# Performance work log

Hardware: AMD Instinct MI355X
Metric: run time of the kernel (lower is better)

## Reference

```python
import jax, jax.numpy as jnp
import numpy as np

B, S, D_MODEL, H = 2, 2048, 512, 8
DH = D_MODEL // H  # dim per head
NEG_INF = 1e9


def setup_inputs() -> dict:
    key = jax.random.key(0)
    ks = jax.random.split(key, 8)
    sc = 0.05
    return {
        "query": jax.random.normal(ks[0], (B, S, D_MODEL), jnp.float32),
        "key": jax.random.normal(ks[1], (B, S, D_MODEL), jnp.float32),
        "value": jax.random.normal(ks[2], (B, S, D_MODEL), jnp.float32),
        "mask": jnp.zeros((B, 1, S, S), jnp.float32),
        "wq": jax.random.normal(ks[3], (D_MODEL, D_MODEL), jnp.float32) * sc,
        "bq": jnp.zeros((D_MODEL,), jnp.float32),
        "wk": jax.random.normal(ks[4], (D_MODEL, D_MODEL), jnp.float32) * sc,
        "bk": jnp.zeros((D_MODEL,), jnp.float32),
        "wv": jax.random.normal(ks[5], (D_MODEL, D_MODEL), jnp.float32) * sc,
        "bv": jnp.zeros((D_MODEL,), jnp.float32),
        "wo": jax.random.normal(ks[6], (D_MODEL, D_MODEL), jnp.float32) * sc,
        "bo": jnp.zeros((D_MODEL,), jnp.float32),
    }


def _split_heads(x):
    # (B, S, D_MODEL) -> (B, H, S, DH)
    b, s, _ = x.shape
    return x.reshape(b, s, H, DH).transpose(0, 2, 1, 3)


def reference(query, key, value, mask, wq, bq, wk, bk, wv, bv, wo, bo):
    q = _split_heads(query @ wq + bq)
    k = _split_heads(key @ wk + bk)
    v = _split_heads(value @ wv + bv)
    # scaled dot-product attention; full (B, H, S, S) scores as in original
    scores = jnp.einsum("bhqd,bhkd->bhqk", q, k) / jnp.sqrt(jnp.float32(DH))
    scores = scores + mask * (-NEG_INF)
    weights = jax.nn.softmax(scores, axis=-1)  # dropout inactive (rate=0 / eval)
    attn = jnp.einsum("bhqk,bhkd->bhqd", weights, v)
    # merge heads: (B, H, S, DH) -> (B, S, D_MODEL)
    b = attn.shape[0]
    merged = attn.transpose(0, 2, 1, 3).reshape(b, -1, D_MODEL)
    return merged @ wo + bo
```

## Files before the change

### kernel.cpp

```cpp
#include <hip/hip_runtime.h>
#include <hip/hip_bf16.h>

typedef unsigned short u16;
typedef unsigned int u32;
typedef __bf16 bf16x8 __attribute__((ext_vector_type(8)));
typedef float f32x4 __attribute__((ext_vector_type(4)));
typedef u16 u16x8 __attribute__((ext_vector_type(8)));
typedef u32 u32x2 __attribute__((ext_vector_type(2)));

#define S_LEN 2048
#define DMODEL 512
#define NHEAD 8
#define DHEAD 64
#define QSCALE 0.1803368801111204f
#define MASKC 1.4426950409e9f
#define RESCALE_THR 8.0f

static __device__ __forceinline__ u16 f2bf(float f) {
    union { float f; unsigned u; } cv; cv.f = f;
    unsigned u = cv.u;
    return (u16)((u + 0x7fffu + ((u >> 16) & 1u)) >> 16);
}
static __device__ __forceinline__ u32 pk2bf(float a, float b) {
    union { __hip_bfloat162 h; u32 u; } cv;
    float2 f2; f2.x = a; f2.y = b;
    cv.h = __float22bfloat162_rn(f2);
    return cv.u;
}
static __device__ __forceinline__ bf16x8 ld8(const u16* p) {
    return *(const bf16x8*)p;
}
static __device__ __forceinline__ float fmax3(float a, float b, float c) {
    return __builtin_fmaxf(__builtin_fmaxf(a, b), c);
}

__global__ __launch_bounds__(256) void prep_kernel(
    const float* __restrict__ q, const float* __restrict__ k, const float* __restrict__ v,
    const float* __restrict__ w0, const float* __restrict__ w1,
    const float* __restrict__ w2, const float* __restrict__ w3,
    const float* __restrict__ mask,
    u16* __restrict__ Aqkv, u16* __restrict__ wtall, int* __restrict__ flags) {
    const int p = blockIdx.x;
    const int tid = threadIdx.x;
    __shared__ float t[32][33];
    __shared__ int wred[4];
    if (p < 3072) {
        const int z = p >> 10, px = p & 1023;
        const float* in = (z == 0) ? q : (z == 1) ? k : v;
        u16* o = Aqkv + (long)z * 2097152;
        long i = ((long)px * 256 + tid) * 8;
        f32x4 a = *(const f32x4*)(in + i);
        f32x4 b = *(const f32x4*)(in + i + 4);
        u16x8 r;
#pragma unroll
        for (int j = 0; j < 4; ++j) { r[j] = f2bf(a[j]); r[4 + j] = f2bf(b[j]); }
        *(u16x8*)(o + i) = r;
    } else if (p < 4096) {
        const int p2 = p - 3072;
        const int z = p2 >> 8, rem = p2 & 255, by = rem >> 4, bx = rem & 15;
        const float* in = (z == 0) ? w0 : (z == 1) ? w1 : (z == 2) ? w2 : w3;
        u16* o = wtall + (long)(((z + 1) & 3)) * 262144;
        const int tx = tid & 31, ty = tid >> 5;
#pragma unroll
        for (int i = 0; i < 4; ++i)
            t[ty + 8 * i][tx] = in[(by * 32 + ty + 8 * i) * DMODEL + bx * 32 + tx];
        __syncthreads();
#pragma unroll
        for (int i = 0; i < 4; ++i)
            o[(bx * 32 + ty + 8 * i) * DMODEL + by * 32 + tx] = f2bf(t[tx][ty + 8 * i]);
    } else {
        const int bid = p - 4096;
        const int b = bid >> 10, qt = (bid >> 5) & 31, kt = bid & 31;
        const int r = tid >> 2, cs = tid & 3;
        const float* mp = mask + ((long)(b * S_LEN + qt * 64 + r)) * S_LEN + kt * 64 + cs * 16;
        int nz = 0;
#pragma unroll
        for (int j = 0; j < 4; ++j) {
            f32x4 a = *(const f32x4*)(mp + j * 4);
            nz |= (a[0] != 0.f) | (a[1] != 0.f) | (a[2] != 0.f) | (a[3] != 0.f);
        }
        unsigned long long ball = __ballot(nz);
        if ((tid & 63) == 0) wred[tid >> 6] = (ball != 0ull) ? 1 : 0;
        __syncthreads();
        if (tid == 0) flags[bid] = wred[0] | wred[1] | wred[2] | wred[3];
    }
}

template <bool F32OUT, int TM>
static __device__ __forceinline__ void gemm_body(const u16* __restrict__ A,
                                                 const u16* __restrict__ Wt,
                                                 const float* __restrict__ bias,
                                                 void* __restrict__ Cp, float oscale,
                                                 bool vtout, int bx, int by) {
    const int lane = threadIdx.x & 63;
    const int wave = threadIdx.x >> 6;
    const int wr = wave >> 1, wc = wave & 1;
    const int m0 = by * (TM * 32) + wr * (TM * 16);
    const int n0 = bx * 64 + wc * 32;
    const int cidx = lane & 15;
    const int kg = lane >> 4;

    const u16* aptr[TM];
    const u16* bptr[2];
#pragma unroll
    for (int t = 0; t < TM; ++t)
        aptr[t] = A + (long)(m0 + t * 16 + cidx) * DMODEL + kg * 8;
#pragma unroll
    for (int t = 0; t < 2; ++t)
        bptr[t] = Wt + (long)(n0 + t * 16 + cidx) * DMODEL + kg * 8;

    const f32x4 fz = {0.f, 0.f, 0.f, 0.f};
    f32x4 acc[TM][2];
#pragma unroll
    for (int i = 0; i < TM; ++i)
#pragma unroll
        for (int j = 0; j < 2; ++j) acc[i][j] = fz;

#pragma unroll 4
    for (int k0 = 0; k0 < 512; k0 += 32) {
        bf16x8 a[TM], b[2];
#pragma unroll
        for (int t = 0; t < TM; ++t) a[t] = ld8(aptr[t] + k0);
#pragma unroll
        for (int t = 0; t < 2; ++t) b[t] = ld8(bptr[t] + k0);
#pragma unroll
        for (int i = 0; i < TM; ++i)
#pragma unroll
            for (int j = 0; j < 2; ++j)
                acc[i][j] = __builtin_amdgcn_mfma_f32_16x16x32_bf16(a[i], b[j], acc[i][j], 0, 0, 0);
    }

    if (vtout) {
        const int bb = m0 >> 11;
#pragma unroll
        for (int j = 0; j < 2; ++j) {
            int col = n0 + j * 16 + cidx;
            float bv = bias[col];
            u16* vt = (u16*)Cp + (((long)(bb * 8 + (col >> 6))) * 64 + (col & 63)) * S_LEN;
#pragma unroll
            for (int i = 0; i < TM; ++i) {
                int s = (m0 + i * 16 + kg * 4) & (S_LEN - 1);
                u32x2 d;
                d[0] = pk2bf(acc[i][j][0] + bv, acc[i][j][1] + bv);
                d[1] = pk2bf(acc[i][j][2] + bv, acc[i][j][3] + bv);
                *(u32x2*)(vt + s) = d;
            }
        }
        return;
    }

#pragma unroll
    for (int j = 0; j < 2; ++j) {
        int col = n0 + j * 16 + cidx;
        float bv = bias[col];
#pragma unroll
        for (int i = 0; i < TM; ++i) {
#pragma unroll
            for (int r = 0; r < 4; ++r) {
                int row = m0 + i * 16 + kg * 4 + r;
                float val = (acc[i][j][r] + bv) * oscale;
                if (F32OUT) {
                    ((float*)Cp)[(long)row * DMODEL + col] = val;
                } else {
                    ((u16*)Cp)[(long)row * DMODEL + col] = f2bf(val);
                }
            }
        }
    }
}

static __device__ __forceinline__ void xcd_swizzle(int gridX, int gridY, int& bx, int& by) {
    const int flat = blockIdx.x + gridX * blockIdx.y;
    const int xcd = flat & 7;
    const int j = flat >> 3;
    by = xcd * (gridY >> 3) + j / gridX;
    bx = j % gridX;
}

__global__ __launch_bounds__(256) void qkv_gemm_kernel(
    const u16* __restrict__ Aqkv,
    const u16* __restrict__ wtall,
    const float* __restrict__ bq, const float* __restrict__ bk, const float* __restrict__ bv,
    u16* __restrict__ Q, u16* __restrict__ K, u16* __restrict__ Vt) {
    const u16* A = Aqkv + (long)blockIdx.z * 2097152;
    const u16* W = wtall + (long)(blockIdx.z + 1) * 262144;
    const float* b;
    u16* C;
    float sc = 1.f;
    bool vt = false;
    if (blockIdx.z == 0) { b = bq; C = Q; sc = QSCALE; }
    else if (blockIdx.z == 1) { b = bk; C = K; }
    else { b = bv; C = Vt; vt = true; }
    int bx, by;
    xcd_swizzle(8, 32, bx, by);
    gemm_body<false, 4>(A, W, b, C, sc, vt, bx, by);
}

__global__ __launch_bounds__(256) void out_gemm_kernel(const u16* __restrict__ A,
                                                       const u16* __restrict__ Wt,
                                                       const float* __restrict__ bias,
                                                       float* __restrict__ C) {
    int bx, by;
    xcd_swizzle(8, 64, bx, by);
    gemm_body<true, 2>(A, Wt, bias, C, 1.f, false, bx, by);
}

__global__ __launch_bounds__(256) void attn_kernel(const u16* __restrict__ Q,
                                                   const u16* __restrict__ K,
                                                   const u16* __restrict__ Vt,
                                                   const float* __restrict__ mask,
                                                   const int* __restrict__ flags,
                                                   u16* __restrict__ Ab) {
    const int tid = threadIdx.x;
    const int lane = tid & 63;
    const int wave = tid >> 6;
    const int cidx = lane & 15;
    const int kg = lane >> 4;
    const int bh = blockIdx.y;
    const int b = bh >> 3, h = bh & 7;
    const int q0 = blockIdx.x * 64 + wave * 16;

    __shared__ u16 kt_lds[2][64 * 64];
    __shared__ u16 vt_lds[2][64 * 64];
    __shared__ u16 p_lds[4][16 * 64];
    u16* pw = p_lds[wave];

    const long qbase = ((long)(b * S_LEN + q0 + cidx)) * DMODEL + h * DHEAD + kg * 8;
    bf16x8 aq0 = ld8(Q + qbase);
    bf16x8 aq1 = ld8(Q + qbase + 32);

    bf16x8 onesf;
    {
        u16x8 t8;
        u16 ob = (cidx == 0) ? (u16)0x3F80 : (u16)0;
#pragma unroll
        for (int j = 0; j < 8; ++j) t8[j] = ob;
        onesf = *(bf16x8*)&t8;
    }

    const f32x4 fz = {0.f, 0.f, 0.f, 0.f};
    f32x4 acc[4];
#pragma unroll
    for (int nt = 0; nt < 4; ++nt) acc[nt] = fz;
    f32x4 accL = fz;
    float mrow = -1e30f;

    const int krow0 = tid >> 3, kseg0 = tid & 7;
    const int krow1 = krow0 + 32;
    const u16* kgbase = K + ((long)(b * S_LEN)) * DMODEL + h * DHEAD;
    const u16* vgbase = Vt + ((long)bh * DHEAD) * S_LEN;
    const int kd0 = krow0 * 64 + (((kseg0 ^ (krow0 & 7))) << 3);
    const int kd1 = krow1 * 64 + (((kseg0 ^ (krow1 & 7))) << 3);
    const int* flagrow = flags + b * 1024 + blockIdx.x * 32;
    const int NIT = S_LEN / 64;

    const u16* kp0 = kgbase + (long)krow0 * DMODEL + kseg0 * 8;
    const u16* kp1 = kgbase + (long)krow1 * DMODEL + kseg0 * 8;
    const u16* vp0 = vgbase + (long)krow0 * S_LEN + kseg0 * 8;
    const u16* vp1 = vgbase + (long)krow1 * S_LEN + kseg0 * 8;

    u16x8 rk0 = *(const u16x8*)kp0;
    u16x8 rk1 = *(const u16x8*)kp1;
    u16x8 rv0 = *(const u16x8*)vp0;
    u16x8 rv1 = *(const u16x8*)vp1;
    *(u16x8*)&kt_lds[0][kd0] = rk0;
    *(u16x8*)&kt_lds[0][kd1] = rk1;
    *(u16x8*)&vt_lds[0][kd0] = rv0;
    *(u16x8*)&vt_lds[0][kd1] = rv1;
    rk0 = *(const u16x8*)(kp0 + 64 * DMODEL);
    rk1 = *(const u16x8*)(kp1 + 64 * DMODEL);
    rv0 = *(const u16x8*)(vp0 + 64);
    rv1 = *(const u16x8*)(vp1 + 64);
    __syncthreads();

    for (int it = 0; it < NIT; ++it) {
        const int cur = it & 1;
        if (it + 1 < NIT) {
            u16* kn = kt_lds[cur ^ 1];
            u16* vn = vt_lds[cur ^ 1];
            *(u16x8*)&kn[kd0] = rk0;
            *(u16x8*)&kn[kd1] = rk1;
            *(u16x8*)&vn[kd0] = rv0;
            *(u16x8*)&vn[kd1] = rv1;
            if (it + 2 < NIT) {
                const int t2 = (it + 2) * 64;
                rk0 = *(const u16x8*)(kp0 + (long)t2 * DMODEL);
                rk1 = *(const u16x8*)(kp1 + (long)t2 * DMODEL);
                rv0 = *(const u16x8*)(vp0 + t2);
                rv1 = *(const u16x8*)(vp1 + t2);
            }
        }
        const int flg = flagrow[it];
        const u16* kb = kt_lds[cur];
        const u16* vb = vt_lds[cur];

        f32x4 sacc[4];
#pragma unroll
        for (int ct = 0; ct < 4; ++ct) sacc[ct] = fz;
        __builtin_amdgcn_s_setprio(1);
#pragma unroll
        for (int ct = 0; ct < 4; ++ct) {
            int r = ct * 16 + cidx;
            bf16x8 kv0 = ld8(&kb[r * 64 + ((kg ^ (r & 7)) << 3)]);
            bf16x8 kv1 = ld8(&kb[r * 64 + (((4 ^ kg) ^ (r & 7)) << 3)]);
            sacc[ct] = __builtin_amdgcn_mfma_f32_16x16x32_bf16(kv0, aq0, sacc[ct], 0, 0, 0);
            sacc[ct] = __builtin_amdgcn_mfma_f32_16x16x32_bf16(kv1, aq1, sacc[ct], 0, 0, 0);
        }
        __builtin_amdgcn_s_setprio(0);
        if (flg) {
            const float* mb = mask + ((long)(b * S_LEN + q0 + cidx)) * S_LEN + it * 64 + kg * 4;
#pragma unroll
            for (int ct = 0; ct < 4; ++ct) {
                f32x4 mv = *(const f32x4*)(mb + ct * 16);
#pragma unroll
                for (int r = 0; r < 4; ++r) sacc[ct][r] -= MASKC * mv[r];
            }
        }
        float t0 = fmax3(sacc[0][0], sacc[0][1], sacc[0][2]);
        float t1 = fmax3(sacc[0][3], sacc[1][0], sacc[1][1]);
        float t2 = fmax3(sacc[1][2], sacc[1][3], sacc[2][0]);
        float t3 = fmax3(sacc[2][1], sacc[2][2], sacc[2][3]);
        float t4 = fmax3(sacc[3][0], sacc[3][1], sacc[3][2]);
        float mxl = __builtin_fmaxf(fmax3(fmax3(t0, t1, t2), t3, t4), sacc[3][3]);
        if (__any(mxl > mrow + RESCALE_THR)) {
            float mx = fmaxf(mxl, __shfl_xor(mxl, 16));
            mx = fmaxf(mx, __shfl_xor(mx, 32));
            float mnew = fmaxf(mrow, mx);
            float alpha = __builtin_amdgcn_exp2f(mrow - mnew);
            mrow = mnew;
            accL = accL * alpha;
#pragma unroll
            for (int nt = 0; nt < 4; ++nt) acc[nt] = acc[nt] * alpha;
        }
#pragma unroll
        for (int ct = 0; ct < 4; ++ct)
#pragma unroll
            for (int r = 0; r < 4; ++r)
                sacc[ct][r] = __builtin_amdgcn_exp2f(sacc[ct][r] - mrow);
#pragma unroll
        for (int ct = 0; ct < 4; ++ct) {
            u32x2 d;
            d[0] = pk2bf(sacc[ct][0], sacc[ct][1]);
            d[1] = pk2bf(sacc[ct][2], sacc[ct][3]);
            int blk = 2 * ct + (kg >> 1);
            *(u32x2*)&pw[cidx * 64 + ((blk ^ (cidx & 7)) << 3) + (kg & 1) * 4] = d;
        }
        bf16x8 pf0 = ld8(&pw[cidx * 64 + ((kg ^ (cidx & 7)) << 3)]);
        bf16x8 pf1 = ld8(&pw[cidx * 64 + (((4 ^ kg) ^ (cidx & 7)) << 3)]);
        __builtin_amdgcn_s_setprio(1);
#pragma unroll
        for (int nt = 0; nt < 4; ++nt) {
            int rr = nt * 16 + cidx;
            bf16x8 v0 = ld8(&vb[rr * 64 + ((kg ^ (rr & 7)) << 3)]);
            bf16x8 v1 = ld8(&vb[rr * 64 + (((4 ^ kg) ^ (rr & 7)) << 3)]);
            acc[nt] = __builtin_amdgcn_mfma_f32_16x16x32_bf16(v0, pf0, acc[nt], 0, 0, 0);
            acc[nt] = __builtin_amdgcn_mfma_f32_16x16x32_bf16(v1, pf1, acc[nt], 0, 0, 0);
        }
        accL = __builtin_amdgcn_mfma_f32_16x16x32_bf16(onesf, pf0, accL, 0, 0, 0);
        accL = __builtin_amdgcn_mfma_f32_16x16x32_bf16(onesf, pf1, accL, 0, 0, 0);
        __builtin_amdgcn_s_setprio(0);
        __syncthreads();
    }
    float Lb = __shfl(accL[0], cidx);
    float invL = 1.f / Lb;
    const long abase = ((long)(b * S_LEN + q0 + cidx)) * DMODEL + h * DHEAD;
#pragma unroll
    for (int nt = 0; nt < 4; ++nt) {
        u32x2 d;
        d[0] = pk2bf(acc[nt][0] * invL, acc[nt][1] * invL);
        d[1] = pk2bf(acc[nt][2] * invL, acc[nt][3] * invL);
        *(u32x2*)(Ab + abase + nt * 16 + kg * 4) = d;
    }
}

extern "C" void kernel_launch(void* const* d_in, const int* in_sizes, int n_in,
                              void* d_out, int out_size, void* d_ws, size_t ws_size,
                              hipStream_t stream) {
    const float* q_in = (const float*)d_in[0];
    const float* k_in = (const float*)d_in[1];
    const float* v_in = (const float*)d_in[2];
    const float* mask = (const float*)d_in[3];
    const float* wq = (const float*)d_in[4];
    const float* bq = (const float*)d_in[5];
    const float* wk = (const float*)d_in[6];
    const float* bk = (const float*)d_in[7];
    const float* wv = (const float*)d_in[8];
    const float* bv = (const float*)d_in[9];
    const float* wo = (const float*)d_in[10];
    const float* bo = (const float*)d_in[11];

    u16* ws = (u16*)d_ws;
    u16* Qb = ws;
    u16* Kb = Qb + 2097152;
    u16* Vt = Kb + 2097152;
    u16* wtall = Vt + 2097152;
    u16* Sreg = wtall + 4 * 262144;
    u16* Ab = Sreg + 3 * 2097152;
    int* mflags = (int*)(Ab + 2097152);

    prep_kernel<<<6144, 256, 0, stream>>>(q_in, k_in, v_in, wq, wk, wv, wo, mask,
                                          Sreg, wtall, mflags);
    qkv_gemm_kernel<<<dim3(8, 32, 3), 256, 0, stream>>>(Sreg, wtall, bq, bk, bv, Qb, Kb, Vt);
    attn_kernel<<<dim3(32, 16), 256, 0, stream>>>(Qb, Kb, Vt, mask, mflags, Ab);
    out_gemm_kernel<<<dim3(8, 64), 256, 0, stream>>>(Ab, wtall, bo, (float*)d_out);
}
```

Baseline: 202.2 us.

## Fuse fp32-to-bf16 input conversion into QKV GEMM, swizzle and unroll attention

Drops the separate activation conversion pass from the prep kernel. The QKV GEMM now reads fp32 inputs directly and packs them to bf16 in registers, removing a bf16 write and re-read of the activations. The attention kernel also remaps block indices in an XCD-aware way and unrolls its tile loop by two with a macro, giving constant double-buffer indices. The trade-off is that the GEMM loads twice the bytes per A fragment and does the conversion redundantly across the N-tile blocks.

```diff
diff --git a/kernel.cpp b/kernel.cpp
--- a/kernel.cpp
+++ b/kernel.cpp
@@ -7,6 +7,7 @@
 typedef float f32x4 __attribute__((ext_vector_type(4)));
 typedef u16 u16x8 __attribute__((ext_vector_type(8)));
 typedef u32 u32x2 __attribute__((ext_vector_type(2)));
+typedef u32 u32x4 __attribute__((ext_vector_type(4)));
 
 #define S_LEN 2048
 #define DMODEL 512
@@ -30,34 +31,29 @@
 static __device__ __forceinline__ bf16x8 ld8(const u16* p) {
     return *(const bf16x8*)p;
 }
+static __device__ __forceinline__ bf16x8 ld8f(const float* p) {
+    f32x4 a = *(const f32x4*)p;
+    f32x4 b = *(const f32x4*)(p + 4);
+    u32x4 w;
+    w[0] = pk2bf(a[0], a[1]); w[1] = pk2bf(a[2], a[3]);
+    w[2] = pk2bf(b[0], b[1]); w[3] = pk2bf(b[2], b[3]);
+    union { u32x4 u; bf16x8 h; } cv; cv.u = w; return cv.h;
+}
 static __device__ __forceinline__ float fmax3(float a, float b, float c) {
     return __builtin_fmaxf(__builtin_fmaxf(a, b), c);
 }
 
 __global__ __launch_bounds__(256) void prep_kernel(
-    const float* __restrict__ q, const float* __restrict__ k, const float* __restrict__ v,
     const float* __restrict__ w0, const float* __restrict__ w1,
     const float* __restrict__ w2, const float* __restrict__ w3,
     const float* __restrict__ mask,
-    u16* __restrict__ Aqkv, u16* __restrict__ wtall, int* __restrict__ flags) {
+    u16* __restrict__ wtall, int* __restrict__ flags) {
     const int p = blockIdx.x;
     const int tid = threadIdx.x;
     __shared__ float t[32][33];
     __shared__ int wred[4];
-    if (p < 3072) {
-        const int z = p >> 10, px = p & 1023;
-        const float* in = (z == 0) ? q : (z == 1) ? k : v;
-        u16* o = Aqkv + (long)z * 2097152;
-        long i = ((long)px * 256 + tid) * 8;
-        f32x4 a = *(const f32x4*)(in + i);
-        f32x4 b = *(const f32x4*)(in + i + 4);
-        u16x8 r;
-#pragma unroll
-        for (int j = 0; j < 4; ++j) { r[j] = f2bf(a[j]); r[4 + j] = f2bf(b[j]); }
-        *(u16x8*)(o + i) = r;
-    } else if (p < 4096) {
-        const int p2 = p - 3072;
-        const int z = p2 >> 8, rem = p2 & 255, by = rem >> 4, bx = rem & 15;
+    if (p < 1024) {
+        const int z = p >> 8, rem = p & 255, by = rem >> 4, bx = rem & 15;
         const float* in = (z == 0) ? w0 : (z == 1) ? w1 : (z == 2) ? w2 : w3;
         u16* o = wtall + (long)(((z + 1) & 3)) * 262144;
         const int tx = tid & 31, ty = tid >> 5;
@@ -69,7 +65,7 @@
         for (int i = 0; i < 4; ++i)
             o[(bx * 32 + ty + 8 * i) * DMODEL + by * 32 + tx] = f2bf(t[tx][ty + 8 * i]);
     } else {
-        const int bid = p - 4096;
+        const int bid = p - 1024;
         const int b = bid >> 10, qt = (bid >> 5) & 31, kt = bid & 31;
         const int r = tid >> 2, cs = tid & 3;
         const float* mp = mask + ((long)(b * S_LEN + qt * 64 + r)) * S_LEN + kt * 64 + cs * 16;
@@ -83,6 +79,49 @@
         if ((tid & 63) == 0) wred[tid >> 6] = (ball != 0ull) ? 1 : 0;
         __syncthreads();
         if (tid == 0) flags[bid] = wred[0] | wred[1] | wred[2] | wred[3];
+    }
+}
+
+template <bool F32OUT, int TM>
+static __device__ __forceinline__ void store_c(f32x4 (&acc)[TM][2],
+                                               const float* __restrict__ bias,
+                                               void* __restrict__ Cp, float oscale,
+                                               bool vtout, int m0, int n0, int cidx, int kg) {
+    if (vtout) {
+        const int bb = m0 >> 11;
+#pragma unroll
+        for (int j = 0; j < 2; ++j) {
+            int col = n0 + j * 16 + cidx;
+            float bv = bias[col];
+            u16* vt = (u16*)Cp + (((long)(bb * 8 + (col >> 6))) * 64 + (col & 63)) * S_LEN;
+#pragma unroll
+            for (int i = 0; i < TM; ++i) {
+                int s = (m0 + i * 16 + kg * 4) & (S_LEN - 1);
+                u32x2 d;
+                d[0] = pk2bf(acc[i][j][0] + bv, acc[i][j][1] + bv);
+                d[1] = pk2bf(acc[i][j][2] + bv, acc[i][j][3] + bv);
+                *(u32x2*)(vt + s) = d;
+            }
+        }
+        return;
+    }
+#pragma unroll
+    for (int j = 0; j < 2; ++j) {
+        int col = n0 + j * 16 + cidx;
+        float bv = bias[col];
+#pragma unroll
+        for (int i = 0; i < TM; ++i) {
+#pragma unroll
+            for (int r = 0; r < 4; ++r) {
+                int row = m0 + i * 16 + kg * 4 + r;
+                float val = (acc[i][j][r] + bv) * oscale;
+                if (F32OUT) {
+                    ((float*)Cp)[(long)row * DMODEL + col] = val;
+                } else {
+                    ((u16*)Cp)[(long)row * DMODEL + col] = f2bf(val);
+                }
+            }
+        }
     }
 }
 
@@ -129,44 +168,53 @@
             for (int j = 0; j < 2; ++j)
                 acc[i][j] = __builtin_amdgcn_mfma_f32_16x16x32_bf16(a[i], b[j], acc[i][j], 0, 0, 0);
     }
-
-    if (vtout) {
-        const int bb = m0 >> 11;
-#pragma unroll
-        for (int j = 0; j < 2; ++j) {
-            int col = n0 + j * 16 + cidx;
-            float bv = bias[col];
-            u16* vt = (u16*)Cp + (((long)(bb * 8 + (col >> 6))) * 64 + (col & 63)) * S_LEN;
-#pragma unroll
-            for (int i = 0; i < TM; ++i) {
-                int s = (m0 + i * 16 + kg * 4) & (S_LEN - 1);
-                u32x2 d;
-                d[0] = pk2bf(acc[i][j][0] + bv, acc[i][j][1] + bv);
-                d[1] = pk2bf(acc[i][j][2] + bv, acc[i][j][3] + bv);
-                *(u32x2*)(vt + s) = d;
-            }
-        }
-        return;
-    }
-
-#pragma unroll
-    for (int j = 0; j < 2; ++j) {
-        int col = n0 + j * 16 + cidx;
-        float bv = bias[col];
-#pragma unroll
-        for (int i = 0; i < TM; ++i) {
-#pragma unroll
-            for (int r = 0; r < 4; ++r) {
-                int row = m0 + i * 16 + kg * 4 + r;
-                float val = (acc[i][j][r] + bv) * oscale;
-                if (F32OUT) {
-                    ((float*)Cp)[(long)row * DMODEL + col] = val;
-                } else {
-                    ((u16*)Cp)[(long)row * DMODEL + col] = f2bf(val);
-                }
-            }
-        }
-    }
+    store_c<F32OUT, TM>(acc, bias, Cp, oscale, vtout, m0, n0, cidx, kg);
+}
+
+template <int TM>
+static __device__ __forceinline__ void gemm_body_af32(const float* __restrict__ A,
+                                                      const u16* __restrict__ Wt,
+                                                      const float* __restrict__ bias,
+                                                      void* __restrict__ Cp, float oscale,
+                                                      bool vtout, int bx, int by) {
+    const int lane = threadIdx.x & 63;
+    const int wave = threadIdx.x >> 6;
+    const int wr = wave >> 1, wc = wave & 1;
+    const int m0 = by * (TM * 32) + wr * (TM * 16);
+    const int n0 = bx * 64 + wc * 32;
+    const int cidx = lane & 15;
+    const int kg = lane >> 4;
+
+    const float* aptr[TM];
+    const u16* bptr[2];
+#pragma unroll
+    for (int t = 0; t < TM; ++t)
+        aptr[t] = A + (long)(m0 + t * 16 + cidx) * DMODEL + kg * 8;
+#pragma unroll
+    for (int t = 0; t < 2; ++t)
+        bptr[t] = Wt + (long)(n0 + t * 16 + cidx) * DMODEL + kg * 8;
+
+    const f32x4 fz = {0.f, 0.f, 0.f, 0.f};
+    f32x4 acc[TM][2];
+#pragma unroll
+    for (int i = 0; i < TM; ++i)
+#pragma unroll
+        for (int j = 0; j < 2; ++j) acc[i][j] = fz;
+
+#pragma unroll 2
+    for (int k0 = 0; k0 < 512; k0 += 32) {
+        bf16x8 a[TM], b[2];
+#pragma unroll
+        for (int t = 0; t < TM; ++t) a[t] = ld8f(aptr[t] + k0);
+#pragma unroll
+        for (int t = 0; t < 2; ++t) b[t] = ld8(bptr[t] + k0);
+#pragma unroll
+        for (int i = 0; i < TM; ++i)
+#pragma unroll
+            for (int j = 0; j < 2; ++j)
+                acc[i][j] = __builtin_amdgcn_mfma_f32_16x16x32_bf16(a[i], b[j], acc[i][j], 0, 0, 0);
+    }
+    store_c<false, TM>(acc, bias, Cp, oscale, vtout, m0, n0, cidx, kg);
 }
 
 static __device__ __forceinline__ void xcd_swizzle(int gridX, int gridY, int& bx, int& by) {
@@ -178,11 +226,11 @@
 }
 
 __global__ __launch_bounds__(256) void qkv_gemm_kernel(
-    const u16* __restrict__ Aqkv,
+    const float* __restrict__ Aq, const float* __restrict__ Ak, const float* __restrict__ Av,
     const u16* __restrict__ wtall,
     const float* __restrict__ bq, const float* __restrict__ bk, const float* __restrict__ bv,
     u16* __restrict__ Q, u16* __restrict__ K, u16* __restrict__ Vt) {
-    const u16* A = Aqkv + (long)blockIdx.z * 2097152;
+    const float* A = (blockIdx.z == 0) ? Aq : (blockIdx.z == 1) ? Ak : Av;
     const u16* W = wtall + (long)(blockIdx.z + 1) * 262144;
     const float* b;
     u16* C;
@@ -193,7 +241,7 @@
     else { b = bv; C = Vt; vt = true; }
     int bx, by;
     xcd_swizzle(8, 32, bx, by);
-    gemm_body<false, 4>(A, W, b, C, sc, vt, bx, by);
+    gemm_body_af32<4>(A, W, b, C, sc, vt, bx, by);
 }
 
 __global__ __launch_bounds__(256) void out_gemm_kernel(const u16* __restrict__ A,
@@ -216,9 +264,12 @@
     const int wave = tid >> 6;
     const int cidx = lane & 15;
     const int kg = lane >> 4;
-    const int bh = blockIdx.y;
+    const int flat = blockIdx.x + 32 * blockIdx.y;
+    const int F = (flat & 7) * 64 + (flat >> 3);
+    const int qt = F & 31;
+    const int bh = F >> 5;
     const int b = bh >> 3, h = bh & 7;
-    const int q0 = blockIdx.x * 64 + wave * 16;
+    const int q0 = qt * 64 + wave * 16;
 
     __shared__ u16 kt_lds[2][64 * 64];
     __shared__ u16 vt_lds[2][64 * 64];
@@ -251,7 +302,7 @@
     const u16* vgbase = Vt + ((long)bh * DHEAD) * S_LEN;
     const int kd0 = krow0 * 64 + (((kseg0 ^ (krow0 & 7))) << 3);
     const int kd1 = krow1 * 64 + (((kseg0 ^ (krow1 & 7))) << 3);
-    const int* flagrow = flags + b * 1024 + blockIdx.x * 32;
+    const int* flagrow = flags + b * 1024 + qt * 32;
     const int NIT = S_LEN / 64;
 
     const u16* kp0 = kgbase + (long)krow0 * DMODEL + kseg0 * 8;
@@ -273,94 +324,100 @@
     rv1 = *(const u16x8*)(vp1 + 64);
     __syncthreads();
 
-    for (int it = 0; it < NIT; ++it) {
-        const int cur = it & 1;
-        if (it + 1 < NIT) {
-            u16* kn = kt_lds[cur ^ 1];
-            u16* vn = vt_lds[cur ^ 1];
-            *(u16x8*)&kn[kd0] = rk0;
-            *(u16x8*)&kn[kd1] = rk1;
-            *(u16x8*)&vn[kd0] = rv0;
-            *(u16x8*)&vn[kd1] = rv1;
-            if (it + 2 < NIT) {
-                const int t2 = (it + 2) * 64;
-                rk0 = *(const u16x8*)(kp0 + (long)t2 * DMODEL);
-                rk1 = *(const u16x8*)(kp1 + (long)t2 * DMODEL);
-                rv0 = *(const u16x8*)(vp0 + t2);
-                rv1 = *(const u16x8*)(vp1 + t2);
-            }
-        }
-        const int flg = flagrow[it];
-        const u16* kb = kt_lds[cur];
-        const u16* vb = vt_lds[cur];
-
-        f32x4 sacc[4];
-#pragma unroll
-        for (int ct = 0; ct < 4; ++ct) sacc[ct] = fz;
-        __builtin_amdgcn_s_setprio(1);
-#pragma unroll
-        for (int ct = 0; ct < 4; ++ct) {
-            int r = ct * 16 + cidx;
-            bf16x8 kv0 = ld8(&kb[r * 64 + ((kg ^ (r & 7)) << 3)]);
-            bf16x8 kv1 = ld8(&kb[r * 64 + (((4 ^ kg) ^ (r & 7)) << 3)]);
-            sacc[ct] = __builtin_amdgcn_mfma_f32_16x16x32_bf16(kv0, aq0, sacc[ct], 0, 0, 0);
-            sacc[ct] = __builtin_amdgcn_mfma_f32_16x16x32_bf16(kv1, aq1, sacc[ct], 0, 0, 0);
-        }
-        __builtin_amdgcn_s_setprio(0);
-        if (flg) {
-            const float* mb = mask + ((long)(b * S_LEN + q0 + cidx)) * S_LEN + it * 64 + kg * 4;
-#pragma unroll
-            for (int ct = 0; ct < 4; ++ct) {
-                f32x4 mv = *(const f32x4*)(mb + ct * 16);
-#pragma unroll
-                for (int r = 0; r < 4; ++r) sacc[ct][r] -= MASKC * mv[r];
-            }
-        }
-        float t0 = fmax3(sacc[0][0], sacc[0][1], sacc[0][2]);
-        float t1 = fmax3(sacc[0][3], sacc[1][0], sacc[1][1]);
-        float t2 = fmax3(sacc[1][2], sacc[1][3], sacc[2][0]);
-        float t3 = fmax3(sacc[2][1], sacc[2][2], sacc[2][3]);
-        float t4 = fmax3(sacc[3][0], sacc[3][1], sacc[3][2]);
-        float mxl = __builtin_fmaxf(fmax3(fmax3(t0, t1, t2), t3, t4), sacc[3][3]);
-        if (__any(mxl > mrow + RESCALE_THR)) {
-            float mx = fmaxf(mxl, __shfl_xor(mxl, 16));
-            mx = fmaxf(mx, __shfl_xor(mx, 32));
-            float mnew = fmaxf(mrow, mx);
-            float alpha = __builtin_amdgcn_exp2f(mrow - mnew);
-            mrow = mnew;
-            accL = accL * alpha;
-#pragma unroll
-            for (int nt = 0; nt < 4; ++nt) acc[nt] = acc[nt] * alpha;
-        }
-#pragma unroll
-        for (int ct = 0; ct < 4; ++ct)
-#pragma unroll
-            for (int r = 0; r < 4; ++r)
-                sacc[ct][r] = __builtin_amdgcn_exp2f(sacc[ct][r] - mrow);
-#pragma unroll
-        for (int ct = 0; ct < 4; ++ct) {
-            u32x2 d;
-            d[0] = pk2bf(sacc[ct][0], sacc[ct][1]);
-            d[1] = pk2bf(sacc[ct][2], sacc[ct][3]);
-            int blk = 2 * ct + (kg >> 1);
-            *(u32x2*)&pw[cidx * 64 + ((blk ^ (cidx & 7)) << 3) + (kg & 1) * 4] = d;
-        }
-        bf16x8 pf0 = ld8(&pw[cidx * 64 + ((kg ^ (cidx & 7)) << 3)]);
-        bf16x8 pf1 = ld8(&pw[cidx * 64 + (((4 ^ kg) ^ (cidx & 7)) << 3)]);
-        __builtin_amdgcn_s_setprio(1);
-#pragma unroll
-        for (int nt = 0; nt < 4; ++nt) {
-            int rr = nt * 16 + cidx;
-            bf16x8 v0 = ld8(&vb[rr * 64 + ((kg ^ (rr & 7)) << 3)]);
-            bf16x8 v1 = ld8(&vb[rr * 64 + (((4 ^ kg) ^ (rr & 7)) << 3)]);
-            acc[nt] = __builtin_amdgcn_mfma_f32_16x16x32_bf16(v0, pf0, acc[nt], 0, 0, 0);
-            acc[nt] = __builtin_amdgcn_mfma_f32_16x16x32_bf16(v1, pf1, acc[nt], 0, 0, 0);
-        }
-        accL = __builtin_amdgcn_mfma_f32_16x16x32_bf16(onesf, pf0, accL, 0, 0, 0);
-        accL = __builtin_amdgcn_mfma_f32_16x16x32_bf16(onesf, pf1, accL, 0, 0, 0);
-        __builtin_amdgcn_s_setprio(0);
-        __syncthreads();
-    }
+#define ATTN_TILE(IT, CUR)                                                                 \
+    {                                                                                      \
+        if ((IT) + 1 < NIT) {                                                              \
+            u16* kn = kt_lds[(CUR) ^ 1];                                                   \
+            u16* vn = vt_lds[(CUR) ^ 1];                                                   \
+            *(u16x8*)&kn[kd0] = rk0;                                                       \
+            *(u16x8*)&kn[kd1] = rk1;                                                       \
+            *(u16x8*)&vn[kd0] = rv0;                                                       \
+            *(u16x8*)&vn[kd1] = rv1;                                                       \
+            if ((IT) + 2 < NIT) {                                                          \
+                const int t2 = ((IT) + 2) * 64;                                            \
+                rk0 = *(const u16x8*)(kp0 + (long)t2 * DMODEL);                            \
+                rk1 = *(const u16x8*)(kp1 + (long)t2 * DMODEL);                            \
+                rv0 = *(const u16x8*)(vp0 + t2);                                           \
+                rv1 = *(const u16x8*)(vp1 + t2);                                           \
+            }                                                                              \
+        }                                                                                  \
+        const int flg = flagrow[(IT)];                                                     \
+        const u16* kb = kt_lds[(CUR)];                                                     \
+        const u16* vb = vt_lds[(CUR)];                                                     \
+        f32x4 sacc[4];                                                                     \
+        _Pragma("unroll")                                                                  \
+        for (int ct = 0; ct < 4; ++ct) sacc[ct] = fz;                                      \
+        __builtin_amdgcn_s_setprio(1);                                                     \
+        _Pragma("unroll")                                                                  \
+        for (int ct = 0; ct < 4; ++ct) {                                                   \
+            int r = ct * 16 + cidx;                                                        \
+            bf16x8 kv0 = ld8(&kb[r * 64 + ((kg ^ (r & 7)) << 3)]);                         \
+            bf16x8 kv1 = ld8(&kb[r * 64 + (((4 ^ kg) ^ (r & 7)) << 3)]);                   \
+            sacc[ct] = __builtin_amdgcn_mfma_f32_16x16x32_bf16(kv0, aq0, sacc[ct], 0, 0, 0); \
+            sacc[ct] = __builtin_amdgcn_mfma_f32_16x16x32_bf16(kv1, aq1, sacc[ct], 0, 0, 0); \
+        }                                                                                  \
+        __builtin_amdgcn_s_setprio(0);                                                     \
+        if (flg) {                                                                         \
+            const float* mb = mask + ((long)(b * S_LEN + q0 + cidx)) * S_LEN + (IT) * 64 + kg * 4; \
+            _Pragma("unroll")                                                              \
+            for (int ct = 0; ct < 4; ++ct) {                                               \
+                f32x4 mv = *(const f32x4*)(mb + ct * 16);                                  \
+                _Pragma("unroll")                                                          \
+                for (int r = 0; r < 4; ++r) sacc[ct][r] -= MASKC * mv[r];                  \
+            }                                                                              \
+        }                                                                                  \
+        float t0 = fmax3(sacc[0][0], sacc[0][1], sacc[0][2]);                              \
+        float t1 = fmax3(sacc[0][3], sacc[1][0], sacc[1][1]);                              \
+        float t2 = fmax3(sacc[1][2], sacc[1][3], sacc[2][0]);                              \
+        float t3 = fmax3(sacc[2][1], sacc[2][2], sacc[2][3]);                              \
+        float t4 = fmax3(sacc[3][0], sacc[3][1], sacc[3][2]);                              \
+        float mxl = __builtin_fmaxf(fmax3(fmax3(t0, t1, t2), t3, t4), sacc[3][3]);         \
+        if (__any(mxl > mrow + RESCALE_THR)) {                                             \
+            float mx = fmaxf(mxl, __shfl_xor(mxl, 16));                                    \
+            mx = fmaxf(mx, __shfl_xor(mx, 32));                                            \
+            float mnew = fmaxf(mrow, mx);                                                  \
+            float alpha = __builtin_amdgcn_exp2f(mrow - mnew);                             \
+            mrow = mnew;                                                                   \
+            accL = accL * alpha;                                                           \
+            _Pragma("unroll")                                                              \
+            for (int nt = 0; nt < 4; ++nt) acc[nt] = acc[nt] * alpha;                      \
+        }                                                                                  \
+        _Pragma("unroll")                                                                  \
+        for (int ct = 0; ct < 4; ++ct)                                                     \
+            _Pragma("unroll")                                                              \
+            for (int r = 0; r < 4; ++r)                                                    \
+                sacc[ct][r] = __builtin_amdgcn_exp2f(sacc[ct][r] - mrow);                  \
+        _Pragma("unroll")                                                                  \
+        for (int ct = 0; ct < 4; ++ct) {                                                   \
+            u32x2 d;                                                                       \
+            d[0] = pk2bf(sacc[ct][0], sacc[ct][1]);                                        \
+            d[1] = pk2bf(sacc[ct][2], sacc[ct][3]);                                        \
+            int blk = 2 * ct + (kg >> 1);                                                  \
+            *(u32x2*)&pw[cidx * 64 + ((blk ^ (cidx & 7)) << 3) + (kg & 1) * 4] = d;        \
+        }                                                                                  \
+        bf16x8 pf0 = ld8(&pw[cidx * 64 + ((kg ^ (cidx & 7)) << 3)]);                       \
+        bf16x8 pf1 = ld8(&pw[cidx * 64 + (((4 ^ kg) ^ (cidx & 7)) << 3)]);                 \
+        __builtin_amdgcn_s_setprio(1);                                                     \
+        _Pragma("unroll")                                                                  \
+        for (int nt = 0; nt < 4; ++nt) {                                                   \
+            int rr = nt * 16 + cidx;                                                       \
+            bf16x8 v0 = ld8(&vb[rr * 64 + ((kg ^ (rr & 7)) << 3)]);                        \
+            bf16x8 v1 = ld8(&vb[rr * 64 + (((4 ^ kg) ^ (rr & 7)) << 3)]);                  \
+            acc[nt] = __builtin_amdgcn_mfma_f32_16x16x32_bf16(v0, pf0, acc[nt], 0, 0, 0);  \
+            acc[nt] = __builtin_amdgcn_mfma_f32_16x16x32_bf16(v1, pf1, acc[nt], 0, 0, 0);  \
+        }                                                                                  \
+        accL = __builtin_amdgcn_mfma_f32_16x16x32_bf16(onesf, pf0, accL, 0, 0, 0);         \
+        accL = __builtin_amdgcn_mfma_f32_16x16x32_bf16(onesf, pf1, accL, 0, 0, 0);         \
+        __builtin_amdgcn_s_setprio(0);                                                     \
+        __syncthreads();                                                                   \
+    }
+
+    for (int it = 0; it < NIT; it += 2) {
+        ATTN_TILE(it, 0)
+        ATTN_TILE(it + 1, 1)
+    }
+#undef ATTN_TILE
+
     float Lb = __shfl(accL[0], cidx);
     float invL = 1.f / Lb;
     const long abase = ((long)(b * S_LEN + q0 + cidx)) * DMODEL + h * DHEAD;
@@ -394,13 +451,12 @@
     u16* Kb = Qb + 2097152;
     u16* Vt = Kb + 2097152;
     u16* wtall = Vt + 2097152;
-    u16* Sreg = wtall + 4 * 262144;
-    u16* Ab = Sreg + 3 * 2097152;
+    u16* Ab = wtall + 4 * 262144;
     int* mflags = (int*)(Ab + 2097152);
 
-    prep_kernel<<<6144, 256, 0, stream>>>(q_in, k_in, v_in, wq, wk, wv, wo, mask,
-                                          Sreg, wtall, mflags);
-    qkv_gemm_kernel<<<dim3(8, 32, 3), 256, 0, stream>>>(Sreg, wtall, bq, bk, bv, Qb, Kb, Vt);
+    prep_kernel<<<3072, 256, 0, stream>>>(wq, wk, wv, wo, mask, wtall, mflags);
+    qkv_gemm_kernel<<<dim3(8, 32, 3), 256, 0, stream>>>(q_in, k_in, v_in, wtall,
+                                                        bq, bk, bv, Qb, Kb, Vt);
     attn_kernel<<<dim3(32, 16), 256, 0, stream>>>(Qb, Kb, Vt, mask, mflags, Ab);
     out_gemm_kernel<<<dim3(8, 64), 256, 0, stream>>>(Ab, wtall, bo, (float*)d_out);
 }
```

Result: slower. 224.0 us (+10.8%).
